# Kernel optimization log

Hardware: AMD Instinct MI355X
Metric: run time of the kernel (lower is better)

Reference implementation:

```python
import jax, jax.numpy as jnp
import numpy as np

EMBED_DIM = 2048
NUM_HEADS = 32
HEAD_DIM = EMBED_DIM // NUM_HEADS  # 64; only used as softmax scale
BATCH = 2
SEQ_LEN = 2048


def setup_inputs() -> dict:
    key = jax.random.key(0)
    ks = jax.random.split(key, 5)
    scale = 1.0 / np.sqrt(EMBED_DIM)
    x = jax.random.normal(ks[0], (BATCH, SEQ_LEN, EMBED_DIM), dtype=jnp.float32)
    Wq = jax.random.normal(ks[1], (EMBED_DIM, EMBED_DIM), dtype=jnp.float32) * scale
    Wk = jax.random.normal(ks[2], (EMBED_DIM, EMBED_DIM), dtype=jnp.float32) * scale
    Wv = jax.random.normal(ks[3], (EMBED_DIM, EMBED_DIM), dtype=jnp.float32) * scale
    Wo = jax.random.normal(ks[4], (EMBED_DIM, EMBED_DIM), dtype=jnp.float32) * scale
    return {"x": x, "Wq": Wq, "Wk": Wk, "Wv": Wv, "Wo": Wo}


def reference(x, Wq, Wk, Wv, Wo):
    # x: [b, s, e]
    q = jnp.einsum('bse,ef->bsf', x, Wq)  # [b, s, e]
    k = jnp.einsum('bse,ef->bsf', x, Wk)
    v = jnp.einsum('bse,ef->bsf', x, Wv)
    # NOTE: original transposes (1,2) WITHOUT splitting heads, so "attention"
    # is over the embed dimension: q^T k -> [b, e, e]
    qT = jnp.swapaxes(q, 1, 2)  # [b, e, s]
    kT = jnp.swapaxes(k, 1, 2)  # [b, e, s]
    vT = jnp.swapaxes(v, 1, 2)  # [b, e, s]
    attn_scores = jnp.einsum('bes,bfs->bef', qT, kT) / np.sqrt(HEAD_DIM)  # [b,e,e]
    attn_weights = jax.nn.softmax(attn_scores, axis=-1)
    attn_output = jnp.einsum('bef,bfs->bes', attn_weights, vT)  # [b, e, s]
    attn_output = jnp.swapaxes(attn_output, 1, 2)  # [b, s, e]
    return jnp.einsum('bse,ef->bsf', attn_output, Wo)
```

## Files before the change

kernel.cpp:

```cpp
#include <hip/hip_runtime.h>
#include <cstddef>
#include <cstdint>

constexpr int E     = 2048;
constexpr int SEQ   = 2048;
constexpr int BATCH = 2;
constexpr int BS    = BATCH * SEQ;

constexpr int BM = 128, BN = 128, BK = 64;

typedef _Float16 f16;
typedef f16  f16x4 __attribute__((ext_vector_type(4)));
typedef f16  f16x8 __attribute__((ext_vector_type(8)));
typedef float f32x4 __attribute__((ext_vector_type(4)));

#define GLOAD16(g, l)                                                   \
    __builtin_amdgcn_global_load_lds(                                   \
        (const __attribute__((address_space(1))) void*)(g),             \
        (__attribute__((address_space(3))) void*)(l), 16, 0, 0)

__device__ __forceinline__ void gemm_core(
    const f16* __restrict__ Ab, const f16* __restrict__ Bb,
    int K, int lda, int ldb, int m0, int n0,
    f16* At, f16* Bt, f32x4 acc[4][4])
{
    const int tid = threadIdx.x;
    const int l  = tid & 63;
    const int w  = tid >> 6;
    const int lr = l & 15;
    const int hi = l >> 4;
    const int wm = (w >> 1) * 64;
    const int wn = (w & 1) * 64;

    auto stage = [&](int buf, int k0) {
#pragma unroll
        for (int p = 0; p < 4; ++p) {
            const int ci  = p * 256 + tid;
            const int row = ci >> 3;
            const int sc  = (ci & 7) ^ (row & 7);
            GLOAD16(Ab + (size_t)(m0 + row) * lda + k0 + sc * 8,
                    At + buf * (BM * BK) + p * 2048 + w * 512);
            GLOAD16(Bb + (size_t)(n0 + row) * ldb + k0 + sc * 8,
                    Bt + buf * (BN * BK) + p * 2048 + w * 512);
        }
    };

    stage(0, 0);
    __syncthreads();

    const int NT = K / BK;
    int cur = 0;
    for (int t = 0; t < NT; ++t) {
        if (t + 1 < NT) stage(cur ^ 1, (t + 1) * BK);

        const f16* Ac = At + cur * (BM * BK);
        const f16* Bc = Bt + cur * (BN * BK);
        f16x8 af[4][2], bf[4][2];
#pragma unroll
        for (int i = 0; i < 4; ++i)
#pragma unroll
            for (int ks = 0; ks < 2; ++ks) {
                const int ar = wm + i * 16 + lr;
                const int ap = (ks * 4 + hi) ^ (ar & 7);
                af[i][ks] = *reinterpret_cast<const f16x8*>(Ac + ar * 64 + ap * 8);
                const int br = wn + i * 16 + lr;
                const int bp = (ks * 4 + hi) ^ (br & 7);
                bf[i][ks] = *reinterpret_cast<const f16x8*>(Bc + br * 64 + bp * 8);
            }
#pragma unroll
        for (int ks = 0; ks < 2; ++ks)
#pragma unroll
            for (int i = 0; i < 4; ++i)
#pragma unroll
                for (int j = 0; j < 4; ++j)
                    acc[i][j] = __builtin_amdgcn_mfma_f32_16x16x32_f16(
                        af[i][ks], bf[j][ks], acc[i][j], 0, 0, 0);

        __syncthreads();
        cur ^= 1;
    }
}

__device__ __forceinline__ void swz_block(int gx, int gy, int& bx, int& by)
{
    const int nwg  = gx * gy;
    const int flat = blockIdx.y * gx + blockIdx.x;
    const int cpx  = nwg >> 3;
    const int swz  = (flat & 7) * cpx + (flat >> 3);
    bx = swz % gx;
    by = swz / gx;
}

template <int EPI, typename CT>
__global__ __launch_bounds__(256) void gemm_f16(
    const f16* __restrict__ A, const f16* __restrict__ B, CT* __restrict__ C,
    int K, int lda, int ldb, int ldc,
    long long sA, long long sB, long long sC, float alpha)
{
    alignas(16) __shared__ f16 At[2 * BM * BK];
    alignas(16) __shared__ f16 Bt[2 * BN * BK];

    int bx, by; swz_block(gridDim.x, gridDim.y, bx, by);
    const int m0 = by * BM, n0 = bx * BN;

    f32x4 acc[4][4] = {};
    gemm_core(A + (size_t)blockIdx.z * sA, B + (size_t)blockIdx.z * sB,
              K, lda, ldb, m0, n0, At, Bt, acc);

    const int l  = threadIdx.x & 63;
    const int w  = threadIdx.x >> 6;
    const int lr = l & 15, hi = l >> 4;
    const int wm = (w >> 1) * 64, wn = (w & 1) * 64;

    if (EPI == 0) {
        CT* Cb = C + (size_t)blockIdx.z * sC;
#pragma unroll
        for (int i = 0; i < 4; ++i)
#pragma unroll
            for (int r = 0; r < 4; ++r) {
                const int row = m0 + wm + i * 16 + hi * 4 + r;
#pragma unroll
                for (int j = 0; j < 4; ++j) {
                    const int col = n0 + wn + j * 16 + lr;
                    Cb[(size_t)row * ldc + col] = (CT)(alpha * acc[i][j][r]);
                }
            }
    } else {
        f16* Cb = (f16*)C;
#pragma unroll
        for (int i = 0; i < 4; ++i) {
            const int rowb = m0 + wm + i * 16 + hi * 4;
            const long long base = ((long long)(rowb >> 11) << 22) + (rowb & 2047);
#pragma unroll
            for (int j = 0; j < 4; ++j) {
                const int col = n0 + wn + j * 16 + lr;
                f16x4 v = {(f16)(alpha * acc[i][j][0]), (f16)(alpha * acc[i][j][1]),
                           (f16)(alpha * acc[i][j][2]), (f16)(alpha * acc[i][j][3])};
                *reinterpret_cast<f16x4*>(Cb + base + (long long)col * 2048) = v;
            }
        }
    }
}

__global__ __launch_bounds__(256) void qkv_f16(
    const f16* __restrict__ xc,
    const f16* __restrict__ WqT, const f16* __restrict__ WkT,
    const f16* __restrict__ WvT,
    f16* __restrict__ QT, f16* __restrict__ KT, f16* __restrict__ V)
{
    alignas(16) __shared__ f16 At[2 * BM * BK];
    alignas(16) __shared__ f16 Bt[2 * BN * BK];

    const int z = blockIdx.z;
    const f16* B = (z == 0) ? WqT : (z == 1) ? WkT : WvT;

    int bx, by; swz_block(gridDim.x, gridDim.y, bx, by);
    const int m0 = by * BM, n0 = bx * BN;

    f32x4 acc[4][4] = {};
    gemm_core(xc, B, E, E, E, m0, n0, At, Bt, acc);

    const int l  = threadIdx.x & 63;
    const int w  = threadIdx.x >> 6;
    const int lr = l & 15, hi = l >> 4;
    const int wm = (w >> 1) * 64, wn = (w & 1) * 64;

    if (z == 2) {
#pragma unroll
        for (int i = 0; i < 4; ++i)
#pragma unroll
            for (int r = 0; r < 4; ++r) {
                const int row = m0 + wm + i * 16 + hi * 4 + r;
#pragma unroll
                for (int j = 0; j < 4; ++j) {
                    const int col = n0 + wn + j * 16 + lr;
                    V[(size_t)row * E + col] = (f16)acc[i][j][r];
                }
            }
    } else {
        f16* Cb = (z == 0) ? QT : KT;
#pragma unroll
        for (int i = 0; i < 4; ++i) {
            const int rowb = m0 + wm + i * 16 + hi * 4;
            const long long base = ((long long)(rowb >> 11) << 22) + (rowb & 2047);
#pragma unroll
            for (int j = 0; j < 4; ++j) {
                const int col = n0 + wn + j * 16 + lr;
                f16x4 v = {(f16)acc[i][j][0], (f16)acc[i][j][1],
                           (f16)acc[i][j][2], (f16)acc[i][j][3]};
                *reinterpret_cast<f16x4*>(Cb + base + (long long)col * 2048) = v;
            }
        }
    }
}

__global__ __launch_bounds__(256) void conv_x_f16(
    const float* __restrict__ x, f16* __restrict__ xc, int n4)
{
    int i = blockIdx.x * 256 + threadIdx.x;
    const int stride = gridDim.x * 256;
    for (; i < n4; i += stride) {
        const float4 v = reinterpret_cast<const float4*>(x)[i];
        f16x4 h = {(f16)v.x, (f16)v.y, (f16)v.z, (f16)v.w};
        reinterpret_cast<f16x4*>(xc)[i] = h;
    }
}

__global__ __launch_bounds__(256) void conv_wT(
    const float* __restrict__ W0, const float* __restrict__ W1,
    const float* __restrict__ W2, const float* __restrict__ W3,
    f16* __restrict__ O0, f16* __restrict__ O1,
    f16* __restrict__ O2, f16* __restrict__ O3)
{
    const float* src; f16* dst;
    switch (blockIdx.z) {
        case 0: src = W0; dst = O0; break;
        case 1: src = W1; dst = O1; break;
        case 2: src = W2; dst = O2; break;
        default: src = W3; dst = O3; break;
    }
    __shared__ f16 t[64][68];
    const int e0 = blockIdx.y * 64, f0 = blockIdx.x * 64;
    const int tid = threadIdx.x;
    const int tf = (tid & 15) * 4;
    const int te = tid >> 4;
#pragma unroll
    for (int p = 0; p < 4; ++p) {
        const int e = te + p * 16;
        const float4 v = *reinterpret_cast<const float4*>(
            &src[(size_t)(e0 + e) * 2048 + f0 + tf]);
        t[tf + 0][e] = (f16)v.x; t[tf + 1][e] = (f16)v.y;
        t[tf + 2][e] = (f16)v.z; t[tf + 3][e] = (f16)v.w;
    }
    __syncthreads();
#pragma unroll
    for (int p = 0; p < 4; ++p) {
        const int f = (tid >> 4) + p * 16;
        const int e = (tid & 15) * 4;
        const f16x4 v = *reinterpret_cast<const f16x4*>(&t[f][e]);
        *reinterpret_cast<f16x4*>(&dst[(size_t)(f0 + f) * 2048 + e0 + e]) = v;
    }
}

__global__ __launch_bounds__(256) void softmax_rows_f16(
    const float* __restrict__ S, f16* __restrict__ A)
{
    const float* row = S + (size_t)blockIdx.x * 2048;
    f16* arow = A + (size_t)blockIdx.x * 2048;
    const int tid = threadIdx.x;

    float4 v0 = reinterpret_cast<const float4*>(row)[tid];
    float4 v1 = reinterpret_cast<const float4*>(row)[tid + 256];

    float m = fmaxf(fmaxf(fmaxf(v0.x, v0.y), fmaxf(v0.z, v0.w)),
                    fmaxf(fmaxf(v1.x, v1.y), fmaxf(v1.z, v1.w)));
#pragma unroll
    for (int off = 32; off > 0; off >>= 1) m = fmaxf(m, __shfl_xor(m, off));

    __shared__ float red[8];
    if ((tid & 63) == 0) red[tid >> 6] = m;
    __syncthreads();
    m = fmaxf(fmaxf(red[0], red[1]), fmaxf(red[2], red[3]));

    v0.x = __expf(v0.x - m); v0.y = __expf(v0.y - m);
    v0.z = __expf(v0.z - m); v0.w = __expf(v0.w - m);
    v1.x = __expf(v1.x - m); v1.y = __expf(v1.y - m);
    v1.z = __expf(v1.z - m); v1.w = __expf(v1.w - m);

    float s = v0.x + v0.y + v0.z + v0.w + v1.x + v1.y + v1.z + v1.w;
#pragma unroll
    for (int off = 32; off > 0; off >>= 1) s += __shfl_xor(s, off);
    if ((tid & 63) == 0) red[4 + (tid >> 6)] = s;
    __syncthreads();
    s = red[4] + red[5] + red[6] + red[7];

    const float inv = 1.0f / s;
    f16x4 a0 = {(f16)(v0.x * inv), (f16)(v0.y * inv), (f16)(v0.z * inv), (f16)(v0.w * inv)};
    f16x4 a1 = {(f16)(v1.x * inv), (f16)(v1.y * inv), (f16)(v1.z * inv), (f16)(v1.w * inv)};
    reinterpret_cast<f16x4*>(arow)[tid]       = a0;
    reinterpret_cast<f16x4*>(arow)[tid + 256] = a1;
}

extern "C" void kernel_launch(void* const* d_in, const int* in_sizes, int n_in,
                              void* d_out, int out_size, void* d_ws, size_t ws_size,
                              hipStream_t stream)
{
    const float* x  = (const float*)d_in[0];
    const float* Wq = (const float*)d_in[1];
    const float* Wk = (const float*)d_in[2];
    const float* Wv = (const float*)d_in[3];
    const float* Wo = (const float*)d_in[4];
    float* out = (float*)d_out;

    f16* ws16 = (f16*)d_ws;
    const size_t MATE = (size_t)BS * E;
    const size_t WMAT = (size_t)E * E;
    f16* xc  = ws16;
    f16* WqT = xc  + MATE;
    f16* WkT = WqT + WMAT;
    f16* WvT = WkT + WMAT;
    f16* WoT = WvT + WMAT;
    f16* QT  = WoT + WMAT;
    f16* KT  = QT  + MATE;
    f16* V   = KT  + MATE;
    float* S = (float*)(V + MATE);
    f16* A   = QT;
    f16* AO  = KT;

    const dim3 blk(256);
    const long long BMATL = (long long)E * E;

    hipLaunchKernelGGL(conv_x_f16, dim3(2048), blk, 0, stream, x, xc, (int)(MATE / 4));
    hipLaunchKernelGGL(conv_wT, dim3(32, 32, 4), blk, 0, stream,
                       Wq, Wk, Wv, Wo, WqT, WkT, WvT, WoT);

    const dim3 gBig(E / BN, BS / BM, 1);
    const dim3 gSq (E / BN, E  / BM, BATCH);

    hipLaunchKernelGGL(qkv_f16, dim3(E / BN, BS / BM, 3), blk, 0, stream,
                       xc, WqT, WkT, WvT, QT, KT, V);

    hipLaunchKernelGGL((gemm_f16<0, float>), gSq, blk, 0, stream,
                       QT, KT, S, SEQ, E, E, E, BMATL, BMATL, BMATL, 0.125f);

    hipLaunchKernelGGL(softmax_rows_f16, dim3(BATCH * E), blk, 0, stream, S, A);

    hipLaunchKernelGGL((gemm_f16<0, f16>), gSq, blk, 0, stream,
                       V, A, AO, E, E, E, E, BMATL, BMATL, BMATL, 1.0f);

    hipLaunchKernelGGL((gemm_f16<0, float>), gBig, blk, 0, stream,
                       AO, WoT, out, E, E, E, E, 0LL, 0LL, 0LL, 1.0f);
}
```

Measured before the change: 389.6 us.

## Switch GEMM core to triple-buffered BK=32 pipeline with explicit vmcnt waits

Replaces the double-buffered BK=64 LDS pipeline with a three-stage ring of BK=32 tiles, prefetching two tiles ahead. It uses explicit s_waitcnt vmcnt counts and raw barriers instead of __syncthreads so global-to-LDS loads can stay in flight across iterations. The LDS swizzle is changed to a 4-chunk XOR pattern for the narrower rows. The aim is to hide global load latency better, at the cost of twice as many barrier pairs per K and hand-tuned wait counts that must match the number of loads issued.

```diff
diff --git a/kernel.cpp b/kernel.cpp
--- a/kernel.cpp
+++ b/kernel.cpp
@@ -7,7 +7,8 @@
 constexpr int BATCH = 2;
 constexpr int BS    = BATCH * SEQ;
 
-constexpr int BM = 128, BN = 128, BK = 64;
+constexpr int BM = 128, BN = 128, BK = 32;
+constexpr int NBUF = 3;
 
 typedef _Float16 f16;
 typedef f16  f16x4 __attribute__((ext_vector_type(4)));
@@ -18,6 +19,14 @@
     __builtin_amdgcn_global_load_lds(                                   \
         (const __attribute__((address_space(1))) void*)(g),             \
         (__attribute__((address_space(3))) void*)(l), 16, 0, 0)
+
+#define VMCNT(n) asm volatile("s_waitcnt vmcnt(" #n ")" ::: "memory")
+#define BARRIER()                                                       \
+    do { asm volatile("" ::: "memory");                                 \
+         __builtin_amdgcn_s_barrier();                                  \
+         asm volatile("" ::: "memory"); } while (0)
+
+__device__ __forceinline__ int swz4(int r) { return (r & 3) ^ ((r >> 2) & 3); }
 
 __device__ __forceinline__ void gemm_core(
     const f16* __restrict__ Ab, const f16* __restrict__ Bb,
@@ -34,50 +43,48 @@
 
     auto stage = [&](int buf, int k0) {
 #pragma unroll
-        for (int p = 0; p < 4; ++p) {
+        for (int p = 0; p < 2; ++p) {
             const int ci  = p * 256 + tid;
-            const int row = ci >> 3;
-            const int sc  = (ci & 7) ^ (row & 7);
-            GLOAD16(Ab + (size_t)(m0 + row) * lda + k0 + sc * 8,
-                    At + buf * (BM * BK) + p * 2048 + w * 512);
-            GLOAD16(Bb + (size_t)(n0 + row) * ldb + k0 + sc * 8,
-                    Bt + buf * (BN * BK) + p * 2048 + w * 512);
+            const int row = ci >> 2;
+            const int lc  = (ci & 3) ^ swz4(row);
+            GLOAD16(Ab + (size_t)(m0 + row) * lda + k0 + lc * 8,
+                    At + buf * 4096 + p * 2048 + w * 512);
+            GLOAD16(Bb + (size_t)(n0 + row) * ldb + k0 + lc * 8,
+                    Bt + buf * 4096 + p * 2048 + w * 512);
         }
     };
 
+    const int NT = K / BK;
     stage(0, 0);
-    __syncthreads();
-
-    const int NT = K / BK;
-    int cur = 0;
+    stage(1, BK);
+
+    int cur = 0, sb = 2;
     for (int t = 0; t < NT; ++t) {
-        if (t + 1 < NT) stage(cur ^ 1, (t + 1) * BK);
-
-        const f16* Ac = At + cur * (BM * BK);
-        const f16* Bc = Bt + cur * (BN * BK);
-        f16x8 af[4][2], bf[4][2];
+        if (t + 2 < NT) { stage(sb, (t + 2) * BK); VMCNT(8); }
+        else if (t + 1 < NT) { VMCNT(4); }
+        else { VMCNT(0); }
+        BARRIER();
+
+        const f16* Ac = At + cur * 4096;
+        const f16* Bc = Bt + cur * 4096;
+        f16x8 af[4], bf[4];
+#pragma unroll
+        for (int i = 0; i < 4; ++i) {
+            const int ar = wm + i * 16 + lr;
+            af[i] = *reinterpret_cast<const f16x8*>(Ac + ar * 32 + (hi ^ swz4(ar)) * 8);
+            const int br = wn + i * 16 + lr;
+            bf[i] = *reinterpret_cast<const f16x8*>(Bc + br * 32 + (hi ^ swz4(br)) * 8);
+        }
 #pragma unroll
         for (int i = 0; i < 4; ++i)
 #pragma unroll
-            for (int ks = 0; ks < 2; ++ks) {
-                const int ar = wm + i * 16 + lr;
-                const int ap = (ks * 4 + hi) ^ (ar & 7);
-                af[i][ks] = *reinterpret_cast<const f16x8*>(Ac + ar * 64 + ap * 8);
-                const int br = wn + i * 16 + lr;
-                const int bp = (ks * 4 + hi) ^ (br & 7);
-                bf[i][ks] = *reinterpret_cast<const f16x8*>(Bc + br * 64 + bp * 8);
-            }
-#pragma unroll
-        for (int ks = 0; ks < 2; ++ks)
-#pragma unroll
-            for (int i = 0; i < 4; ++i)
-#pragma unroll
-                for (int j = 0; j < 4; ++j)
-                    acc[i][j] = __builtin_amdgcn_mfma_f32_16x16x32_f16(
-                        af[i][ks], bf[j][ks], acc[i][j], 0, 0, 0);
-
-        __syncthreads();
-        cur ^= 1;
+            for (int j = 0; j < 4; ++j)
+                acc[i][j] = __builtin_amdgcn_mfma_f32_16x16x32_f16(
+                    af[i], bf[j], acc[i][j], 0, 0, 0);
+
+        BARRIER();
+        cur = (cur == NBUF - 1) ? 0 : cur + 1;
+        sb  = (sb  == NBUF - 1) ? 0 : sb  + 1;
     }
 }
 
@@ -97,8 +104,8 @@
     int K, int lda, int ldb, int ldc,
     long long sA, long long sB, long long sC, float alpha)
 {
-    alignas(16) __shared__ f16 At[2 * BM * BK];
-    alignas(16) __shared__ f16 Bt[2 * BN * BK];
+    alignas(16) __shared__ f16 At[NBUF * BM * BK];
+    alignas(16) __shared__ f16 Bt[NBUF * BN * BK];
 
     int bx, by; swz_block(gridDim.x, gridDim.y, bx, by);
     const int m0 = by * BM, n0 = bx * BN;
@@ -148,8 +155,8 @@
     const f16* __restrict__ WvT,
     f16* __restrict__ QT, f16* __restrict__ KT, f16* __restrict__ V)
 {
-    alignas(16) __shared__ f16 At[2 * BM * BK];
-    alignas(16) __shared__ f16 Bt[2 * BN * BK];
+    alignas(16) __shared__ f16 At[NBUF * BM * BK];
+    alignas(16) __shared__ f16 Bt[NBUF * BN * BK];
 
     const int z = blockIdx.z;
     const f16* B = (z == 0) ? WqT : (z == 1) ? WkT : WvT;
```

Result: slower. 420.1 us (+7.8%).
